# Kernel optimization log

Hardware: AMD Instinct MI355X
Metric: run time of the kernel (lower is better)

## Reference

```python
import jax, jax.numpy as jnp
import numpy as np

NUM_EMBEDDINGS = 512
EMBEDDING_DIM = 64
COMMITMENT_COST = 0.25


def setup_inputs() -> dict:
    key = jax.random.key(0)
    k1, k2 = jax.random.split(key)
    inputs = jax.random.normal(k1, (32, EMBEDDING_DIM, 64, 64), dtype=jnp.float32)  # NCHW
    lim = 1.0 / NUM_EMBEDDINGS
    weight = jax.random.uniform(k2, (NUM_EMBEDDINGS, EMBEDDING_DIM), dtype=jnp.float32,
                                minval=-lim, maxval=lim)
    return {"inputs": inputs, "weight": weight}


def reference(inputs, weight):
    # NCHW -> NHWC, flatten to [N, D]
    x = jnp.transpose(inputs, (0, 2, 3, 1))  # [B,H,W,D]
    input_shape = x.shape
    flat = x.reshape(-1, EMBEDDING_DIM)  # [N,D]

    distances = (jnp.sum(flat ** 2, axis=1, keepdims=True)
                 + jnp.sum(weight ** 2, axis=1)
                 - 2.0 * flat @ weight.T)  # [N,K]
    encoding_indices = jnp.argmin(distances, axis=1)  # [N]
    encodings = jax.nn.one_hot(encoding_indices, NUM_EMBEDDINGS, dtype=jnp.float32)  # [N,K]

    # gather (equivalent to encodings @ weight)
    quantized = weight[encoding_indices].reshape(input_shape)  # [B,H,W,D]

    e_latent_loss = jnp.mean((jax.lax.stop_gradient(quantized) - x) ** 2)
    q_latent_loss = jnp.mean((quantized - jax.lax.stop_gradient(x)) ** 2)
    loss = q_latent_loss + COMMITMENT_COST * e_latent_loss

    # straight-through estimator
    quantized_st = x + jax.lax.stop_gradient(quantized - x)

    avg_probs = jnp.mean(encodings, axis=0)  # [K]
    perplexity = jnp.exp(-jnp.sum(avg_probs * jnp.log(avg_probs + 1e-10)))

    out = jnp.transpose(quantized_st, (0, 3, 1, 2))  # back to NCHW
    return (loss, out, perplexity, encodings)
```

## Files before the change

### kernel.cpp

```cpp
#include <hip/hip_runtime.h>

typedef short   bf16x8 __attribute__((ext_vector_type(8)));
typedef float   f32x4  __attribute__((ext_vector_type(4)));

#define NVEC   131072
#define HW     4096
#define CHW    262144
#define QOFF   1
#define PERPOFF 8388609
#define ENCOFF  8388610


__device__ inline unsigned short f2bf(float f) {
    unsigned int u = __float_as_uint(f);
    u += 0x7fffu + ((u >> 16) & 1u);
    return (unsigned short)(u >> 16);
}

__global__ __launch_bounds__(64) void vq_prep(const float* __restrict__ wt,
                                              float* __restrict__ bias,
                                              unsigned short* __restrict__ wbf,
                                              int* __restrict__ counts,
                                              double* __restrict__ loss) {
    int c = blockIdx.x, d = threadIdx.x;
    if (c == 0) {
#pragma unroll
        for (int i = 0; i < 8; ++i) counts[d * 8 + i] = 0;
        if (d == 0) loss[0] = 0.0;
    }
    float v = wt[c * 64 + d];
    wbf[c * 64 + d] = f2bf(v);
    float s = v * v;
    for (int off = 32; off; off >>= 1) s += __shfl_down(s, off, 64);
    if (d == 0) bias[c] = -0.5f * s;
}

__global__ __launch_bounds__(512) void vq_assign(
    const float* __restrict__ x, const float* __restrict__ wt,
    const float* __restrict__ bias, const unsigned short* __restrict__ wbf,
    float* __restrict__ out, float* __restrict__ enc,
    int* __restrict__ counts, double* __restrict__ loss_acc)
{
    __shared__ unsigned short wl[512 * 64];
    __shared__ float  biasl[512];
    __shared__ int    hc[512];
    __shared__ int    winners[256];
    __shared__ double lred[8];

    const int t = threadIdx.x, b = blockIdx.x;
    const int batch  = b >> 4;
    const int posblk = (b & 15) << 8;

    {
        const ulonglong2* src = (const ulonglong2*)wbf;
#pragma unroll
        for (int i = 0; i < 8; ++i) {
            int u  = t + 512 * i;
            int c  = u >> 3;
            int bo = (u & 7) << 4;
            ulonglong2 v = src[u];
            *(ulonglong2*)((char*)wl + ((c << 7) | (bo ^ ((c & 7) << 4)))) = v;
        }
        biasl[t] = bias[t];
        hc[t] = 0;
    }
    __syncthreads();

    const int wv = t >> 6, l = t & 63;
    const int g  = l >> 4, cl = l & 15;
    const int posw = posblk + (wv << 5);
    const int d0 = g << 3;

    float xs[2][16];
    const float* xb = x + (size_t)batch * CHW + posw + cl;
#pragma unroll
    for (int s = 0; s < 2; ++s)
#pragma unroll
        for (int j = 0; j < 8; ++j) {
            xs[s][j]     = xb[(size_t)(d0 + j) * HW + 16 * s];
            xs[s][j + 8] = xb[(size_t)(32 + d0 + j) * HW + 16 * s];
        }

    bf16x8 af[2][2];
#pragma unroll
    for (int s = 0; s < 2; ++s)
#pragma unroll
        for (int h = 0; h < 2; ++h)
#pragma unroll
            for (int i = 0; i < 8; ++i)
                af[s][h][i] = (short)f2bf(xs[s][8 * h + i]);

    float best[2][4]; int bidx[2][4];
#pragma unroll
    for (int s = 0; s < 2; ++s)
#pragma unroll
        for (int i = 0; i < 4; ++i) { best[s][i] = -1e30f; bidx[s][i] = 0; }

    const char* wlb = (const char*)wl;
#pragma unroll 4
    for (int tt = 0; tt < 32; ++tt) {
        int c  = (tt << 4) + cl;
        int rb = c << 7;
        int sw = (c & 7) << 4;
        bf16x8 b0 = *(const bf16x8*)(wlb + (rb | ((16 * g) ^ sw)));
        bf16x8 b1 = *(const bf16x8*)(wlb + (rb | ((64 + 16 * g) ^ sw)));
        float bs = biasl[c];
#pragma unroll
        for (int s = 0; s < 2; ++s) {
            f32x4 acc = {bs, bs, bs, bs};
            acc = __builtin_amdgcn_mfma_f32_16x16x32_bf16(af[s][0], b0, acc, 0, 0, 0);
            acc = __builtin_amdgcn_mfma_f32_16x16x32_bf16(af[s][1], b1, acc, 0, 0, 0);
#pragma unroll
            for (int i = 0; i < 4; ++i)
                if (acc[i] > best[s][i]) { best[s][i] = acc[i]; bidx[s][i] = c; }
        }
    }

#pragma unroll
    for (int s = 0; s < 2; ++s)
#pragma unroll
        for (int i = 0; i < 4; ++i) {
            float bd = best[s][i]; int bi = bidx[s][i];
#pragma unroll
            for (int off = 1; off < 16; off <<= 1) {
                float od = __shfl_xor(bd, off, 64);
                int   oi = __shfl_xor(bi, off, 64);
                if (od > bd || (od == bd && oi < bi)) { bd = od; bi = oi; }
            }
            bidx[s][i] = bi;
        }

    if (cl == 0) {
#pragma unroll
        for (int s = 0; s < 2; ++s)
#pragma unroll
            for (int i = 0; i < 4; ++i) {
                int w = bidx[s][i];
                winners[(wv << 5) + (s << 4) + (g << 2) + i] = w;
                atomicAdd(&hc[w], 1);
            }
    }
    __syncthreads();

    float* outb = out + QOFF + (size_t)batch * CHW + posw + cl;
    float ls = 0.f;
#pragma unroll
    for (int s = 0; s < 2; ++s) {
        int widx = winners[(wv << 5) + (s << 4) + cl];
        float q[16];
        *(float4*)&q[0]  = *(const float4*)(wt + widx * 64 + d0);
        *(float4*)&q[4]  = *(const float4*)(wt + widx * 64 + d0 + 4);
        *(float4*)&q[8]  = *(const float4*)(wt + widx * 64 + 32 + d0);
        *(float4*)&q[12] = *(const float4*)(wt + widx * 64 + 32 + d0 + 4);
#pragma unroll
        for (int j = 0; j < 8; ++j) {
            float da = q[j]     - xs[s][j];
            float db = q[j + 8] - xs[s][j + 8];
            ls += da * da + db * db;
            outb[(size_t)(d0 + j) * HW + 16 * s]      = xs[s][j]     + da;
            outb[(size_t)(32 + d0 + j) * HW + 16 * s] = xs[s][j + 8] + db;
        }
    }

    if (t < 256) {
        int widx = winners[t];
        size_t row = (size_t)batch * 4096 + posblk + t;
        enc[row * 512 + widx] = 1.0f;
    }

    double lsd = (double)ls;
    for (int off = 32; off; off >>= 1) lsd += __shfl_down(lsd, off, 64);
    if (l == 0) lred[wv] = lsd;
    __syncthreads();
    if (t == 0) {
        double s = 0.0;
#pragma unroll
        for (int i = 0; i < 8; ++i) s += lred[i];
        atomicAdd(loss_acc, s);
    }

    int v0 = hc[t];
    if (v0) atomicAdd(&counts[t], v0);
}

__global__ __launch_bounds__(512) void vq_fin(const int* __restrict__ counts,
                                              const double* __restrict__ loss_acc,
                                              float* __restrict__ out) {
    __shared__ double red[512];
    int k = threadIdx.x;
    double p = (double)counts[k] * (1.0 / 131072.0);
    red[k] = p * log(p + 1e-10);
    __syncthreads();
    for (int s = 256; s; s >>= 1) {
        if (k < s) red[k] += red[k + s];
        __syncthreads();
    }
    if (k == 0) {
        out[PERPOFF] = (float)exp(-red[0]);
        out[0] = (float)(loss_acc[0] * 1.25 / 8388608.0);
    }
}

extern "C" void kernel_launch(void* const* d_in, const int* in_sizes, int n_in,
                              void* d_out, int out_size, void* d_ws, size_t ws_size,
                              hipStream_t stream) {
    const float* x  = (const float*)d_in[0];
    const float* wt = (const float*)d_in[1];
    float* out = (float*)d_out;
    char* ws = (char*)d_ws;

    int*            counts = (int*)ws;
    double*         loss   = (double*)(ws + 2048);
    float*          bias   = (float*)(ws + 4096);
    unsigned short* wbf    = (unsigned short*)(ws + 8192);
    float*          enc    = out + ENCOFF;

    vq_prep<<<512, 64, 0, stream>>>(wt, bias, wbf, counts, loss);
    hipMemsetAsync((void*)enc, 0, (size_t)NVEC * 512 * sizeof(float), stream);
    vq_assign<<<512, 512, 0, stream>>>(x, wt, bias, wbf, out, enc, counts, loss);
    vq_fin<<<1, 512, 0, stream>>>(counts, loss, out);
}
```

Before: 95.07 us.

## Fuse one-hot encoding writes into assign kernel, drop separate memset

Removes the hipMemsetAsync over the 256 MB one-hot encodings buffer. The assign kernel now writes every full encoding row itself, zeros and the single one, using vectorized float2 nontemporal stores. The quantized output stores also become nontemporal, and launch bounds ask for 4 blocks per CU. This avoids a separate full pass plus a scattered write over the encodings, but puts the large store stream inside the compute kernel, where it could lower overlap or raise register pressure.

```diff
diff --git a/kernel.cpp b/kernel.cpp
--- a/kernel.cpp
+++ b/kernel.cpp
@@ -2,6 +2,7 @@
 
 typedef short   bf16x8 __attribute__((ext_vector_type(8)));
 typedef float   f32x4  __attribute__((ext_vector_type(4)));
+typedef float   f32x2  __attribute__((ext_vector_type(2)));
 
 #define NVEC   131072
 #define HW     4096
@@ -35,11 +36,11 @@
     if (d == 0) bias[c] = -0.5f * s;
 }
 
-__global__ __launch_bounds__(512) void vq_assign(
+__global__ __launch_bounds__(512, 4) void vq_assign(
     const float* __restrict__ x, const float* __restrict__ wt,
     const float* __restrict__ bias, const unsigned short* __restrict__ wbf,
-    float* __restrict__ out, float* __restrict__ enc,
-    int* __restrict__ counts, double* __restrict__ loss_acc)
+    float* __restrict__ out, int* __restrict__ counts,
+    double* __restrict__ loss_acc)
 {
     __shared__ unsigned short wl[512 * 64];
     __shared__ float  biasl[512];
@@ -157,15 +158,9 @@
             float da = q[j]     - xs[s][j];
             float db = q[j + 8] - xs[s][j + 8];
             ls += da * da + db * db;
-            outb[(size_t)(d0 + j) * HW + 16 * s]      = xs[s][j]     + da;
-            outb[(size_t)(32 + d0 + j) * HW + 16 * s] = xs[s][j + 8] + db;
-        }
-    }
-
-    if (t < 256) {
-        int widx = winners[t];
-        size_t row = (size_t)batch * 4096 + posblk + t;
-        enc[row * 512 + widx] = 1.0f;
+            __builtin_nontemporal_store(xs[s][j]     + da, &outb[(size_t)(d0 + j) * HW + 16 * s]);
+            __builtin_nontemporal_store(xs[s][j + 8] + db, &outb[(size_t)(32 + d0 + j) * HW + 16 * s]);
+        }
     }
 
     double lsd = (double)ls;
@@ -178,9 +173,25 @@
         for (int i = 0; i < 8; ++i) s += lred[i];
         atomicAdd(loss_acc, s);
     }
-
     int v0 = hc[t];
     if (v0) atomicAdd(&counts[t], v0);
+
+    {
+        f32x2* encp = (f32x2*)(out + ENCOFF);
+        size_t rowq = ((size_t)batch * 4096 + posw) * 256;
+#pragma unroll 4
+        for (int r = 0; r < 32; ++r, rowq += 256) {
+            int id = winners[(wv << 5) + r];
+#pragma unroll
+            for (int p = 0; p < 4; ++p) {
+                int k = (l + (p << 6)) << 1;
+                f32x2 v;
+                v.x = (k == id)     ? 1.f : 0.f;
+                v.y = (k + 1 == id) ? 1.f : 0.f;
+                __builtin_nontemporal_store(v, &encp[rowq + l + (p << 6)]);
+            }
+        }
+    }
 }
 
 __global__ __launch_bounds__(512) void vq_fin(const int* __restrict__ counts,
@@ -213,10 +224,8 @@
     double*         loss   = (double*)(ws + 2048);
     float*          bias   = (float*)(ws + 4096);
     unsigned short* wbf    = (unsigned short*)(ws + 8192);
-    float*          enc    = out + ENCOFF;
 
     vq_prep<<<512, 64, 0, stream>>>(wt, bias, wbf, counts, loss);
-    hipMemsetAsync((void*)enc, 0, (size_t)NVEC * 512 * sizeof(float), stream);
-    vq_assign<<<512, 512, 0, stream>>>(x, wt, bias, wbf, out, enc, counts, loss);
+    vq_assign<<<512, 512, 0, stream>>>(x, wt, bias, wbf, out, counts, loss);
     vq_fin<<<1, 512, 0, stream>>>(counts, loss, out);
 }
```

After: 133.7 us. 1.41x slower.

## Pack argmax index into score bits and split x into bf16 hi/lo halves

Applied to the files above, without the earlier changes.

Converts x to bf16 by truncating to the high 16 bits and keeps the low halves in packed registers, so the full fp32 value can be rebuilt for the output and loss without holding 32 floats per thread. The argmax now packs the inverted code index into the low 9 bits of each score and does a single unsigned max, in both the MFMA loop and the shuffle reduction. A +4 bias offset keeps scores positive so the unsigned compare orders them correctly. A launch-bounds occupancy hint is added. The risks are truncation instead of round-to-nearest for bf16, and ties or near-ties within the low 9 mantissa bits may pick a different code than the reference.

```diff
diff --git a/kernel.cpp b/kernel.cpp
--- a/kernel.cpp
+++ b/kernel.cpp
@@ -32,10 +32,10 @@
     wbf[c * 64 + d] = f2bf(v);
     float s = v * v;
     for (int off = 32; off; off >>= 1) s += __shfl_down(s, off, 64);
-    if (d == 0) bias[c] = -0.5f * s;
-}
-
-__global__ __launch_bounds__(512) void vq_assign(
+    if (d == 0) bias[c] = 4.0f - 0.5f * s;
+}
+
+__global__ __launch_bounds__(512, 4) void vq_assign(
     const float* __restrict__ x, const float* __restrict__ wt,
     const float* __restrict__ bias, const unsigned short* __restrict__ wbf,
     float* __restrict__ out, float* __restrict__ enc,
@@ -71,30 +71,28 @@
     const int posw = posblk + (wv << 5);
     const int d0 = g << 3;
 
-    float xs[2][16];
+    union AFU { unsigned u[4]; bf16x8 v; };
+    AFU af[2][2]; unsigned lo[2][2][4];
     const float* xb = x + (size_t)batch * CHW + posw + cl;
 #pragma unroll
     for (int s = 0; s < 2; ++s)
 #pragma unroll
-        for (int j = 0; j < 8; ++j) {
-            xs[s][j]     = xb[(size_t)(d0 + j) * HW + 16 * s];
-            xs[s][j + 8] = xb[(size_t)(32 + d0 + j) * HW + 16 * s];
-        }
-
-    bf16x8 af[2][2];
+        for (int h = 0; h < 2; ++h) {
+            int dbase = (h ? 32 : 0) + d0;
+#pragma unroll
+            for (int k = 0; k < 4; ++k) {
+                unsigned u0 = __float_as_uint(xb[(size_t)(dbase + 2 * k)     * HW + 16 * s]);
+                unsigned u1 = __float_as_uint(xb[(size_t)(dbase + 2 * k + 1) * HW + 16 * s]);
+                af[s][h].u[k] = (u1 & 0xffff0000u) | (u0 >> 16);
+                lo[s][h][k]   = (u1 << 16)         | (u0 & 0xffffu);
+            }
+        }
+
+    unsigned best[2][4];
 #pragma unroll
     for (int s = 0; s < 2; ++s)
 #pragma unroll
-        for (int h = 0; h < 2; ++h)
-#pragma unroll
-            for (int i = 0; i < 8; ++i)
-                af[s][h][i] = (short)f2bf(xs[s][8 * h + i]);
-
-    float best[2][4]; int bidx[2][4];
-#pragma unroll
-    for (int s = 0; s < 2; ++s)
-#pragma unroll
-        for (int i = 0; i < 4; ++i) { best[s][i] = -1e30f; bidx[s][i] = 0; }
+        for (int i = 0; i < 4; ++i) best[s][i] = 0u;
 
     const char* wlb = (const char*)wl;
 #pragma unroll 4
@@ -105,14 +103,17 @@
         bf16x8 b0 = *(const bf16x8*)(wlb + (rb | ((16 * g) ^ sw)));
         bf16x8 b1 = *(const bf16x8*)(wlb + (rb | ((64 + 16 * g) ^ sw)));
         float bs = biasl[c];
+        unsigned tag = 511u - (unsigned)c;
 #pragma unroll
         for (int s = 0; s < 2; ++s) {
             f32x4 acc = {bs, bs, bs, bs};
-            acc = __builtin_amdgcn_mfma_f32_16x16x32_bf16(af[s][0], b0, acc, 0, 0, 0);
-            acc = __builtin_amdgcn_mfma_f32_16x16x32_bf16(af[s][1], b1, acc, 0, 0, 0);
-#pragma unroll
-            for (int i = 0; i < 4; ++i)
-                if (acc[i] > best[s][i]) { best[s][i] = acc[i]; bidx[s][i] = c; }
+            acc = __builtin_amdgcn_mfma_f32_16x16x32_bf16(af[s][0].v, b0, acc, 0, 0, 0);
+            acc = __builtin_amdgcn_mfma_f32_16x16x32_bf16(af[s][1].v, b1, acc, 0, 0, 0);
+#pragma unroll
+            for (int i = 0; i < 4; ++i) {
+                unsigned e = (__float_as_uint(acc[i]) & ~511u) | tag;
+                if (e > best[s][i]) best[s][i] = e;
+            }
         }
     }
 
@@ -120,14 +121,13 @@
     for (int s = 0; s < 2; ++s)
 #pragma unroll
         for (int i = 0; i < 4; ++i) {
-            float bd = best[s][i]; int bi = bidx[s][i];
+            unsigned bd = best[s][i];
 #pragma unroll
             for (int off = 1; off < 16; off <<= 1) {
-                float od = __shfl_xor(bd, off, 64);
-                int   oi = __shfl_xor(bi, off, 64);
-                if (od > bd || (od == bd && oi < bi)) { bd = od; bi = oi; }
-            }
-            bidx[s][i] = bi;
+                unsigned od = (unsigned)__shfl_xor((int)bd, off, 64);
+                if (od > bd) bd = od;
+            }
+            best[s][i] = bd;
         }
 
     if (cl == 0) {
@@ -135,7 +135,7 @@
         for (int s = 0; s < 2; ++s)
 #pragma unroll
             for (int i = 0; i < 4; ++i) {
-                int w = bidx[s][i];
+                int w = 511 - (int)(best[s][i] & 511u);
                 winners[(wv << 5) + (s << 4) + (g << 2) + i] = w;
                 atomicAdd(&hc[w], 1);
             }
@@ -147,18 +147,23 @@
 #pragma unroll
     for (int s = 0; s < 2; ++s) {
         int widx = winners[(wv << 5) + (s << 4) + cl];
-        float q[16];
-        *(float4*)&q[0]  = *(const float4*)(wt + widx * 64 + d0);
-        *(float4*)&q[4]  = *(const float4*)(wt + widx * 64 + d0 + 4);
-        *(float4*)&q[8]  = *(const float4*)(wt + widx * 64 + 32 + d0);
-        *(float4*)&q[12] = *(const float4*)(wt + widx * 64 + 32 + d0 + 4);
-#pragma unroll
-        for (int j = 0; j < 8; ++j) {
-            float da = q[j]     - xs[s][j];
-            float db = q[j + 8] - xs[s][j + 8];
-            ls += da * da + db * db;
-            outb[(size_t)(d0 + j) * HW + 16 * s]      = xs[s][j]     + da;
-            outb[(size_t)(32 + d0 + j) * HW + 16 * s] = xs[s][j + 8] + db;
+#pragma unroll
+        for (int h = 0; h < 2; ++h) {
+            int dbase = (h ? 32 : 0) + d0;
+            float qarr[8];
+            *(float4*)&qarr[0] = *(const float4*)(wt + widx * 64 + dbase);
+            *(float4*)&qarr[4] = *(const float4*)(wt + widx * 64 + dbase + 4);
+#pragma unroll
+            for (int k = 0; k < 4; ++k) {
+                unsigned a = af[s][h].u[k], ld = lo[s][h][k];
+                float x0 = __uint_as_float(((a & 0xffffu) << 16) | (ld & 0xffffu));
+                float x1 = __uint_as_float((a & 0xffff0000u)     | (ld >> 16));
+                float da = qarr[2 * k]     - x0;
+                float db = qarr[2 * k + 1] - x1;
+                ls += da * da + db * db;
+                outb[(size_t)(dbase + 2 * k)     * HW + 16 * s] = x0 + da;
+                outb[(size_t)(dbase + 2 * k + 1) * HW + 16 * s] = x1 + db;
+            }
         }
     }
 
```

Result: faster. 91.42 us (-3.8%).
